# Optimization experiments

Hardware: AMD Instinct MI355X
Metric: run time of the kernel (lower is better)

Reference implementation:

```python
import jax, jax.numpy as jnp
import numpy as np

B, S, E, H = 4, 2048, 1024, 16
D = E // H  # head dim = 64
NEG = -1e9


def setup_inputs() -> dict:
    key = jax.random.key(0)
    ks = jax.random.split(key, 6)
    scale = 1.0 / np.sqrt(E)
    return {
        "x": jax.random.normal(ks[0], (B, S, E), dtype=jnp.float32),
        "in_proj_weight": jax.random.normal(ks[1], (3 * E, E), dtype=jnp.float32) * scale,
        "in_proj_bias": jax.random.normal(ks[2], (3 * E,), dtype=jnp.float32) * 0.02,
        "out_proj_weight": jax.random.normal(ks[3], (E, E), dtype=jnp.float32) * scale,
        "out_proj_bias": jax.random.normal(ks[4], (E,), dtype=jnp.float32) * 0.02,
        "mask": jax.random.randint(ks[5], (B, S), 0, 2, dtype=jnp.int32),
    }


def reference(x, in_proj_weight, in_proj_bias, out_proj_weight, out_proj_bias, mask):
    # Equivalent of F.multi_head_attention_forward(h,h,h,...) with batch-first x.
    # qkv projection: [B,S,3E]
    qkv = jnp.einsum("bse,fe->bsf", x, in_proj_weight) + in_proj_bias
    q, k, v = jnp.split(qkv, 3, axis=-1)
    # split heads -> [B,S,H,D]
    q = q.reshape(B, S, H, D) * (1.0 / np.sqrt(D))
    k = k.reshape(B, S, H, D)
    v = v.reshape(B, S, H, D)
    # scores [B,H,Sq,Sk]
    scores = jnp.einsum("bqhd,bkhd->bhqk", q, k)
    # key_padding_mask = (mask == 0): True positions are excluded
    pad = (mask == 0)[:, None, None, :]  # [B,1,1,Sk]
    scores = jnp.where(pad, NEG, scores)
    attn = jax.nn.softmax(scores, axis=-1)
    # attention output -> [B,S,E]
    ctx = jnp.einsum("bhqk,bkhd->bqhd", attn, v).reshape(B, S, E)
    h_ = jnp.einsum("bse,fe->bsf", ctx, out_proj_weight) + out_proj_bias
    # residual; dropout is identity in eval mode
    return x + h_
```

## Files before the change

kernel.cpp:

```cpp
#include <hip/hip_runtime.h>
#include <stdint.h>
#include <math.h>

#define B_ 4
#define S_ 2048
#define E_ 1024
#define H_ 16
#define D_ 64
#define M_ (B_*S_)

typedef __attribute__((ext_vector_type(8))) short bf16x8;
typedef __attribute__((ext_vector_type(4))) float f32x4;

__device__ __forceinline__ unsigned short f2bf(float f) {
  union { float f; uint32_t u; } v; v.f = f;
  uint32_t u = v.u;
  return (unsigned short)((u + 0x7FFFu + ((u >> 16) & 1u)) >> 16);
}

__device__ __forceinline__ void gload16(const void* g, void* l) {
  __builtin_amdgcn_global_load_lds(
      (__attribute__((address_space(1))) void*)g,
      (__attribute__((address_space(3))) void*)l, 16, 0, 0);
}

__device__ __forceinline__ uint32_t cvtpk(float lo, float hi) {
  uint32_t r;
  asm("v_cvt_pk_bf16_f32 %0, %1, %2" : "=v"(r) : "v"(lo), "v"(hi));
  return r;
}

#define N1 ((M_*E_)/4)
#define N2 ((3*E_*E_)/4)
#define N3 ((E_*E_)/4)
#define NM ((B_*S_)/4)
__global__ __launch_bounds__(256) void cvt_all(const float* __restrict__ x,
                                               const float* __restrict__ w1,
                                               const float* __restrict__ w2,
                                               const int* __restrict__ mask,
                                               unsigned short* __restrict__ dst,
                                               float* __restrict__ maskf) {
  int i = blockIdx.x * 256 + threadIdx.x;
  if (i < N1 + N2 + N3) {
    const float* src;
    int j;
    if (i < N1) { src = x; j = i; }
    else if (i < N1 + N2) { src = w1; j = i - N1; }
    else { src = w2; j = i - N1 - N2; }
    float4 v = reinterpret_cast<const float4*>(src)[j];
    ushort4 o;
    o.x = f2bf(v.x); o.y = f2bf(v.y); o.z = f2bf(v.z); o.w = f2bf(v.w);
    reinterpret_cast<ushort4*>(dst)[i] = o;
  } else if (i < N1 + N2 + N3 + NM) {
    int j = i - (N1 + N2 + N3);
    int4 m = reinterpret_cast<const int4*>(mask)[j];
    float4 o;
    o.x = m.x ? 0.0f : -2.0e9f;
    o.y = m.y ? 0.0f : -2.0e9f;
    o.z = m.z ? 0.0f : -2.0e9f;
    o.w = m.w ? 0.0f : -2.0e9f;
    reinterpret_cast<float4*>(maskf)[j] = o;
  }
}

__global__ __launch_bounds__(256) void gemm_qkv128(
    const unsigned short* __restrict__ A,
    const unsigned short* __restrict__ W,
    const float* __restrict__ bias,
    unsigned short* __restrict__ Qg,
    unsigned short* __restrict__ Kg,
    unsigned short* __restrict__ Vtg)
{
  __shared__ __align__(16) unsigned short SMEM[128*136];
  unsigned short* As = SMEM;
  unsigned short* Bs = SMEM + 4096;
  const int tid = threadIdx.x;
  const int lane = tid & 63;
  const int wave = tid >> 6;
  const int wm = (wave >> 1) * 64, wn = (wave & 1) * 64;
  const int l15 = lane & 15, lg = lane >> 4;

  const int orig = blockIdx.y * 24 + blockIdx.x;
  const int xcd = orig & 7;
  const int idx = orig >> 3;
  const int tn = (xcd * 3 + (idx % 3)) * 128;
  const int tm = (idx / 3) * 128;

  f32x4 zero4 = {0.f, 0.f, 0.f, 0.f};
  f32x4 acc[4][4];
  #pragma unroll
  for (int mi = 0; mi < 4; ++mi)
    #pragma unroll
    for (int ni = 0; ni < 4; ++ni) acc[mi][ni] = zero4;

  const int r0 = tid >> 2, c0 = (tid & 3) * 8;
  const unsigned short* Arow0 = A + (size_t)(tm + r0) * E_ + c0;
  const unsigned short* Arow1 = A + (size_t)(tm + r0 + 64) * E_ + c0;
  const unsigned short* Wrow0 = W + (size_t)(tn + r0) * E_ + c0;
  const unsigned short* Wrow1 = W + (size_t)(tn + r0 + 64) * E_ + c0;
  unsigned short* lA0 = As + tid * 8;
  unsigned short* lA1 = As + (tid + 256) * 8;
  unsigned short* lB0 = Bs + tid * 8;
  unsigned short* lB1 = Bs + (tid + 256) * 8;

  for (int k0 = 0; k0 < E_; k0 += 32) {
    gload16(Arow0 + k0, lA0);
    gload16(Arow1 + k0, lA1);
    gload16(Wrow0 + k0, lB0);
    gload16(Wrow1 + k0, lB1);
    __syncthreads();
    bf16x8 af[4], bfm[4];
    #pragma unroll
    for (int mi = 0; mi < 4; ++mi)
      af[mi] = *(const bf16x8*)&As[(wm + mi*16 + l15)*32 + lg*8];
    #pragma unroll
    for (int ni = 0; ni < 4; ++ni)
      bfm[ni] = *(const bf16x8*)&Bs[(wn + ni*16 + l15)*32 + lg*8];
    #pragma unroll
    for (int mi = 0; mi < 4; ++mi)
      #pragma unroll
      for (int ni = 0; ni < 4; ++ni)
        acc[mi][ni] = __builtin_amdgcn_mfma_f32_16x16x32_bf16(af[mi], bfm[ni], acc[mi][ni], 0, 0, 0);
    __syncthreads();
  }

  const int sec = tn >> 10;
  if (sec < 2) {
    #pragma unroll
    for (int ni = 0; ni < 4; ++ni) {
      const int col = tn + wn + ni*16 + l15;
      const float bcol = bias[col];
      const int f2 = col & 1023;
      const int h = f2 >> 6, d = f2 & 63;
      #pragma unroll
      for (int mi = 0; mi < 4; ++mi) {
        #pragma unroll
        for (int r = 0; r < 4; ++r) {
          const int row = tm + wm + mi*16 + lg*4 + r;
          const int b = row >> 11, s = row & (S_-1);
          const size_t bh = (size_t)(b * H_ + h);
          float val = acc[mi][ni][r] + bcol;
          if (sec == 0) {
            Qg[(bh*S_ + s)*D_ + d] = f2bf(val * 0.18033688f);
          } else {
            const int ch = (d >> 3) ^ (s & 7);
            Kg[(bh*S_ + s)*D_ + ch*8 + (d & 7)] = f2bf(val);
          }
        }
      }
    }
  } else {
    __syncthreads();
    unsigned short* T = SMEM;
    #pragma unroll
    for (int ni = 0; ni < 4; ++ni) {
      const int f = wn + ni*16 + l15;
      const float bcol = bias[tn + f];
      #pragma unroll
      for (int mi = 0; mi < 4; ++mi) {
        const int s0 = wm + mi*16 + lg*4;
        uint2 p;
        p.x = cvtpk(acc[mi][ni][0] + bcol, acc[mi][ni][1] + bcol);
        p.y = cvtpk(acc[mi][ni][2] + bcol, acc[mi][ni][3] + bcol);
        *reinterpret_cast<uint2*>(&T[f*136 + s0]) = p;
      }
    }
    __syncthreads();
    const int f = tid >> 1, sch = tid & 1;
    const int d = f & 63, hl = f >> 6;
    const int h = ((tn & 1023) >> 6) + hl;
    const int b = tm >> 11;
    const size_t bh = (size_t)(b * H_ + h);
    const int sbase = (tm & (S_-1)) + sch*64;
    unsigned short* vout = Vtg + (bh*D_ + d)*S_ + sbase;
    const unsigned short* tin = &T[f*136 + sch*64];
    #pragma unroll
    for (int j = 0; j < 8; ++j) {
      uint4 v = *reinterpret_cast<const uint4*>(&tin[j*8]);
      *reinterpret_cast<uint4*>(&vout[(j ^ (d & 7))*8]) = v;
    }
  }
}

__global__ __launch_bounds__(512, 4) void attn_fwd(
    const unsigned short* __restrict__ Qg,
    const unsigned short* __restrict__ Kg,
    const unsigned short* __restrict__ Vtg,
    const float* __restrict__ maskf,
    unsigned short* __restrict__ ctx)
{
  __shared__ __align__(16) unsigned short Ks[2][4096];
  __shared__ __align__(16) unsigned short Vs[2][4096];
  const int tid = threadIdx.x, lane = tid & 63, wave = tid >> 6;
  const int l15 = lane & 15, lg = lane >> 4;
  const int bh = blockIdx.y, b = bh >> 4, h = bh & 15;
  const int q0 = blockIdx.x * 256 + wave * 32;
  const unsigned short* Qb = Qg + (size_t)bh * S_ * D_;
  const unsigned short* Kb = Kg + (size_t)bh * S_ * D_;
  const unsigned short* Vb = Vtg + (size_t)bh * D_ * S_;
  const float* mrow = maskf + b * S_;

  bf16x8 qf[2][2];
  #pragma unroll
  for (int mi = 0; mi < 2; ++mi)
    #pragma unroll
    for (int kc = 0; kc < 2; ++kc)
      qf[mi][kc] = *(const bf16x8*)&Qb[(size_t)(q0 + mi*16 + l15)*D_ + kc*32 + lg*8];

  f32x4 zero4 = {0.f, 0.f, 0.f, 0.f};
  f32x4 accO[2][4];
  f32x4 accL[2] = {zero4, zero4};
  #pragma unroll
  for (int mi = 0; mi < 2; ++mi)
    #pragma unroll
    for (int df = 0; df < 4; ++df) accO[mi][df] = zero4;

  union { uint32_t u[4]; bf16x8 v; } ou;
  ou.u[0] = ou.u[1] = ou.u[2] = ou.u[3] = 0x3F803F80u;
  const bf16x8 onesv = ou.v;

  int kboff0[4], kboff1[4], vboff0[4], vboff1[4];
  #pragma unroll
  for (int kt = 0; kt < 4; ++kt) {
    const int krow = kt*16 + l15;
    kboff0[kt] = (krow*64 + ((lg ^ (krow & 7))*8)) * 2;
    kboff1[kt] = (krow*64 + (((4+lg) ^ (krow & 7))*8)) * 2;
  }
  #pragma unroll
  for (int df = 0; df < 4; ++df) {
    const int vrow = df*16 + l15;
    vboff0[df] = (vrow*64 + ((lg ^ (vrow & 7))*8)) * 2;
    vboff1[df] = (vrow*64 + (((4+lg) ^ (vrow & 7))*8)) * 2;
  }
  const char* KsB = (const char*)&Ks[0][0];
  const char* VsB = (const char*)&Vs[0][0];

  const int sr0 = tid >> 3, sc0 = (tid & 7) * 8;

  gload16(Kb + (size_t)sr0 * D_ + sc0, &Ks[0][tid*8]);
  gload16(Vb + (size_t)sr0 * S_ + sc0, &Vs[0][tid*8]);
  f32x4 mv0[4], mv1[4];
  #pragma unroll
  for (int kt = 0; kt < 4; ++kt)
    mv0[kt] = *(const f32x4*)&mrow[kt*16 + lg*4];
  const unsigned short* kpre = Kb + (size_t)(64 + sr0) * D_ + sc0;
  const unsigned short* vpre = Vb + (size_t)sr0 * S_ + 64 + sc0;
  const float* mpre = mrow + 64 + lg*4;
  __syncthreads();

#define ATTN_TILE(CUR, MVC, MVN, DO_PF)                                         \
  {                                                                             \
    if (DO_PF) {                                                                \
      gload16(kpre, &Ks[(CUR)^1][tid*8]);                                       \
      gload16(vpre, &Vs[(CUR)^1][tid*8]);                                       \
      kpre += 64*D_; vpre += 64;                                                \
      _Pragma("unroll")                                                         \
      for (int kt = 0; kt < 4; ++kt)                                            \
        MVN[kt] = *(const f32x4*)&mpre[kt*16];                                  \
      mpre += 64;                                                               \
    }                                                                           \
    f32x4 s_[2][4];                                                             \
    __builtin_amdgcn_s_setprio(1);                                              \
    _Pragma("unroll")                                                           \
    for (int kt = 0; kt < 4; ++kt) {                                            \
      bf16x8 kf0 = *(const bf16x8*)(KsB + (CUR)*8192 + kboff0[kt]);             \
      bf16x8 kf1 = *(const bf16x8*)(KsB + (CUR)*8192 + kboff1[kt]);             \
      s_[0][kt] = __builtin_amdgcn_mfma_f32_16x16x32_bf16(kf0, qf[0][0], MVC[kt], 0, 0, 0); \
      s_[0][kt] = __builtin_amdgcn_mfma_f32_16x16x32_bf16(kf1, qf[0][1], s_[0][kt], 0, 0, 0); \
      s_[1][kt] = __builtin_amdgcn_mfma_f32_16x16x32_bf16(kf0, qf[1][0], MVC[kt], 0, 0, 0); \
      s_[1][kt] = __builtin_amdgcn_mfma_f32_16x16x32_bf16(kf1, qf[1][1], s_[1][kt], 0, 0, 0); \
    }                                                                           \
    __builtin_amdgcn_s_setprio(0);                                              \
    _Pragma("unroll")                                                           \
    for (int mi = 0; mi < 2; ++mi)                                              \
      _Pragma("unroll")                                                         \
      for (int kt = 0; kt < 4; ++kt)                                            \
        _Pragma("unroll")                                                       \
        for (int r = 0; r < 4; ++r)                                             \
          s_[mi][kt][r] = __builtin_amdgcn_exp2f(s_[mi][kt][r]);                \
    bf16x8 pa[2][2];                                                            \
    _Pragma("unroll")                                                           \
    for (int mi = 0; mi < 2; ++mi) {                                            \
      _Pragma("unroll")                                                         \
      for (int kk = 0; kk < 2; ++kk) {                                          \
        uint32_t a0 = cvtpk(s_[mi][2*kk][0],   s_[mi][2*kk][1]);                \
        uint32_t c1 = cvtpk(s_[mi][2*kk][2],   s_[mi][2*kk][3]);                \
        uint32_t b0 = cvtpk(s_[mi][2*kk+1][0], s_[mi][2*kk+1][1]);              \
        uint32_t d1 = cvtpk(s_[mi][2*kk+1][2], s_[mi][2*kk+1][3]);              \
        asm("v_permlane32_swap_b32 %0, %1" : "+v"(a0), "+v"(b0));               \
        asm("v_permlane16_swap_b32 %0, %1" : "+v"(a0), "+v"(b0));               \
        asm("v_permlane32_swap_b32 %0, %1" : "+v"(c1), "+v"(d1));               \
        asm("v_permlane16_swap_b32 %0, %1" : "+v"(c1), "+v"(d1));               \
        union { bf16x8 v; uint32_t u[4]; } w;                                   \
        w.u[0] = a0; w.u[1] = c1; w.u[2] = b0; w.u[3] = d1;                     \
        pa[mi][kk] = w.v;                                                       \
      }                                                                         \
    }                                                                           \
    __builtin_amdgcn_s_setprio(1);                                              \
    accL[0] = __builtin_amdgcn_mfma_f32_16x16x32_bf16(pa[0][0], onesv, accL[0], 0, 0, 0); \
    accL[1] = __builtin_amdgcn_mfma_f32_16x16x32_bf16(pa[1][0], onesv, accL[1], 0, 0, 0); \
    _Pragma("unroll")                                                           \
    for (int df = 0; df < 4; ++df) {                                            \
      bf16x8 vf = *(const bf16x8*)(VsB + (CUR)*8192 + vboff0[df]);              \
      accO[0][df] = __builtin_amdgcn_mfma_f32_16x16x32_bf16(pa[0][0], vf, accO[0][df], 0, 0, 0); \
      accO[1][df] = __builtin_amdgcn_mfma_f32_16x16x32_bf16(pa[1][0], vf, accO[1][df], 0, 0, 0); \
    }                                                                           \
    accL[0] = __builtin_amdgcn_mfma_f32_16x16x32_bf16(pa[0][1], onesv, accL[0], 0, 0, 0); \
    accL[1] = __builtin_amdgcn_mfma_f32_16x16x32_bf16(pa[1][1], onesv, accL[1], 0, 0, 0); \
    _Pragma("unroll")                                                           \
    for (int df = 0; df < 4; ++df) {                                            \
      bf16x8 vf = *(const bf16x8*)(VsB + (CUR)*8192 + vboff1[df]);              \
      accO[0][df] = __builtin_amdgcn_mfma_f32_16x16x32_bf16(pa[0][1], vf, accO[0][df], 0, 0, 0); \
      accO[1][df] = __builtin_amdgcn_mfma_f32_16x16x32_bf16(pa[1][1], vf, accO[1][df], 0, 0, 0); \
    }                                                                           \
    __builtin_amdgcn_s_setprio(0);                                              \
    __syncthreads();                                                            \
  }

  for (int tt = 0; tt < 32; tt += 2) {
    ATTN_TILE(0, mv0, mv1, 1)
    ATTN_TILE(1, mv1, mv0, (tt < 30))
  }
#undef ATTN_TILE

  #pragma unroll
  for (int mi = 0; mi < 2; ++mi) {
    #pragma unroll
    for (int r = 0; r < 4; ++r) {
      const float iv = 1.0f / accL[mi][r];
      const int srow = q0 + mi*16 + lg*4 + r;
      #pragma unroll
      for (int df = 0; df < 4; ++df) {
        const int d = df*16 + l15;
        ctx[((size_t)b*S_ + srow)*E_ + h*D_ + d] = f2bf(accO[mi][df][r] * iv);
      }
    }
  }
}

__global__ __launch_bounds__(256) void gemm_out(
    const unsigned short* __restrict__ A,
    const unsigned short* __restrict__ W,
    const float* __restrict__ bias,
    const float* __restrict__ xres,
    float* __restrict__ out)
{
  __shared__ __align__(16) unsigned short As[128*32];
  __shared__ __align__(16) unsigned short Bs[128*32];
  const int tid = threadIdx.x;
  const int lane = tid & 63;
  const int wave = tid >> 6;
  const int wm = (wave >> 1) * 64, wn = (wave & 1) * 64;
  const int tm = blockIdx.y * 128, tn = blockIdx.x * 128;
  const int l15 = lane & 15, lg = lane >> 4;

  f32x4 zero4 = {0.f, 0.f, 0.f, 0.f};
  f32x4 acc[4][4];
  #pragma unroll
  for (int mi = 0; mi < 4; ++mi)
    #pragma unroll
    for (int ni = 0; ni < 4; ++ni) acc[mi][ni] = zero4;

  const int r0 = tid >> 2, c0 = (tid & 3) * 8;
  const unsigned short* Arow0 = A + (size_t)(tm + r0) * E_ + c0;
  const unsigned short* Arow1 = A + (size_t)(tm + r0 + 64) * E_ + c0;
  const unsigned short* Wrow0 = W + (size_t)(tn + r0) * E_ + c0;
  const unsigned short* Wrow1 = W + (size_t)(tn + r0 + 64) * E_ + c0;
  unsigned short* lA0 = As + tid * 8;
  unsigned short* lA1 = As + (tid + 256) * 8;
  unsigned short* lB0 = Bs + tid * 8;
  unsigned short* lB1 = Bs + (tid + 256) * 8;

  for (int k0 = 0; k0 < E_; k0 += 32) {
    gload16(Arow0 + k0, lA0);
    gload16(Arow1 + k0, lA1);
    gload16(Wrow0 + k0, lB0);
    gload16(Wrow1 + k0, lB1);
    __syncthreads();
    bf16x8 af[4], bfm[4];
    #pragma unroll
    for (int mi = 0; mi < 4; ++mi)
      af[mi] = *(const bf16x8*)&As[(wm + mi*16 + l15)*32 + lg*8];
    #pragma unroll
    for (int ni = 0; ni < 4; ++ni)
      bfm[ni] = *(const bf16x8*)&Bs[(wn + ni*16 + l15)*32 + lg*8];
    #pragma unroll
    for (int mi = 0; mi < 4; ++mi)
      #pragma unroll
      for (int ni = 0; ni < 4; ++ni)
        acc[mi][ni] = __builtin_amdgcn_mfma_f32_16x16x32_bf16(af[mi], bfm[ni], acc[mi][ni], 0, 0, 0);
    __syncthreads();
  }

  #pragma unroll
  for (int ni = 0; ni < 4; ++ni) {
    const int col = tn + wn + ni*16 + l15;
    const float bcol = bias[col];
    #pragma unroll
    for (int mi = 0; mi < 4; ++mi) {
      #pragma unroll
      for (int r = 0; r < 4; ++r) {
        const int row = tm + wm + mi*16 + lg*4 + r;
        out[(size_t)row*E_ + col] = xres[(size_t)row*E_ + col] + acc[mi][ni][r] + bcol;
      }
    }
  }
}

extern "C" void kernel_launch(void* const* d_in, const int* in_sizes, int n_in,
                              void* d_out, int out_size, void* d_ws, size_t ws_size,
                              hipStream_t stream) {
  const float* x  = (const float*)d_in[0];
  const float* w1 = (const float*)d_in[1];
  const float* b1 = (const float*)d_in[2];
  const float* w2 = (const float*)d_in[3];
  const float* b2 = (const float*)d_in[4];
  const int* mask = (const int*)d_in[5];
  float* out = (float*)d_out;

  const size_t SZ = (size_t)B_*H_*S_*D_;
  unsigned short* Qg  = (unsigned short*)d_ws;
  unsigned short* Kg  = Qg + SZ;
  unsigned short* Vtg = Kg + SZ;
  unsigned short* xb  = Vtg + SZ;
  unsigned short* w1b = xb + (size_t)M_*E_;
  unsigned short* w2b = w1b + (size_t)3*E_*E_;
  float* maskf = (float*)(w2b + (size_t)E_*E_);
  unsigned short* ctx = xb;

  const int ntot = N1 + N2 + N3 + NM;
  cvt_all<<<(ntot + 255)/256, 256, 0, stream>>>(x, w1, w2, mask, xb, maskf);

  gemm_qkv128<<<dim3(24, 64), 256, 0, stream>>>(xb, w1b, b1, Qg, Kg, Vtg);
  attn_fwd<<<dim3(S_/256, B_*H_), 512, 0, stream>>>(Qg, Kg, Vtg, maskf, ctx);
  gemm_out<<<dim3(E_/128, M_/128), 256, 0, stream>>>(ctx, w2b, b2, x, out);
}
```

Baseline: 226.4 us.

## Stage attention output through LDS for coalesced stores and remap blocks across XCDs

The attention epilogue now writes normalized bf16 outputs into a padded per-wave LDS tile and then stores 16-byte vectors per lane, replacing the scattered 2-byte global writes. The grid becomes 1D and the block index is remapped so that the 8 query tiles of one batch-head land on the same XCD under round-robin dispatch, improving L2 reuse of K/V. Shared memory grows to 36 KB to hold the staging buffer, which may affect occupancy under launch_bounds(512,4).

```diff
diff --git a/kernel.cpp b/kernel.cpp
--- a/kernel.cpp
+++ b/kernel.cpp
@@ -189,12 +189,18 @@
     const float* __restrict__ maskf,
     unsigned short* __restrict__ ctx)
 {
-  __shared__ __align__(16) unsigned short Ks[2][4096];
-  __shared__ __align__(16) unsigned short Vs[2][4096];
+  __shared__ __align__(16) unsigned char SMEM[36864];
+  unsigned short* KsP = (unsigned short*)SMEM;
+  unsigned short* VsP = (unsigned short*)(SMEM + 16384);
   const int tid = threadIdx.x, lane = tid & 63, wave = tid >> 6;
   const int l15 = lane & 15, lg = lane >> 4;
-  const int bh = blockIdx.y, b = bh >> 4, h = bh & 15;
-  const int q0 = blockIdx.x * 256 + wave * 32;
+
+  const int lin = blockIdx.x;
+  const int bh = (lin & 7) * 8 + (lin >> 6);
+  const int qi = (lin >> 3) & 7;
+  const int b = bh >> 4, h = bh & 15;
+  const int q0 = qi * 256 + wave * 32;
+
   const unsigned short* Qb = Qg + (size_t)bh * S_ * D_;
   const unsigned short* Kb = Kg + (size_t)bh * S_ * D_;
   const unsigned short* Vb = Vtg + (size_t)bh * D_ * S_;
@@ -232,13 +238,13 @@
     vboff0[df] = (vrow*64 + ((lg ^ (vrow & 7))*8)) * 2;
     vboff1[df] = (vrow*64 + (((4+lg) ^ (vrow & 7))*8)) * 2;
   }
-  const char* KsB = (const char*)&Ks[0][0];
-  const char* VsB = (const char*)&Vs[0][0];
+  const char* KsB = (const char*)KsP;
+  const char* VsB = (const char*)VsP;
 
   const int sr0 = tid >> 3, sc0 = (tid & 7) * 8;
 
-  gload16(Kb + (size_t)sr0 * D_ + sc0, &Ks[0][tid*8]);
-  gload16(Vb + (size_t)sr0 * S_ + sc0, &Vs[0][tid*8]);
+  gload16(Kb + (size_t)sr0 * D_ + sc0, KsP + tid*8);
+  gload16(Vb + (size_t)sr0 * S_ + sc0, VsP + tid*8);
   f32x4 mv0[4], mv1[4];
   #pragma unroll
   for (int kt = 0; kt < 4; ++kt)
@@ -251,8 +257,8 @@
 #define ATTN_TILE(CUR, MVC, MVN, DO_PF)                                         \
   {                                                                             \
     if (DO_PF) {                                                                \
-      gload16(kpre, &Ks[(CUR)^1][tid*8]);                                       \
-      gload16(vpre, &Vs[(CUR)^1][tid*8]);                                       \
+      gload16(kpre, KsP + ((CUR)^1)*4096 + tid*8);                              \
+      gload16(vpre, VsP + ((CUR)^1)*4096 + tid*8);                              \
       kpre += 64*D_; vpre += 64;                                                \
       _Pragma("unroll")                                                         \
       for (int kt = 0; kt < 4; ++kt)                                            \
@@ -323,17 +329,28 @@
   }
 #undef ATTN_TILE
 
+  unsigned short* T = (unsigned short*)SMEM + wave * 2304;
   #pragma unroll
   for (int mi = 0; mi < 2; ++mi) {
     #pragma unroll
     for (int r = 0; r < 4; ++r) {
       const float iv = 1.0f / accL[mi][r];
-      const int srow = q0 + mi*16 + lg*4 + r;
-      #pragma unroll
-      for (int df = 0; df < 4; ++df) {
-        const int d = df*16 + l15;
-        ctx[((size_t)b*S_ + srow)*E_ + h*D_ + d] = f2bf(accO[mi][df][r] * iv);
-      }
+      const int q = mi*16 + lg*4 + r;
+      #pragma unroll
+      for (int df = 0; df < 4; ++df)
+        T[q*72 + df*16 + l15] = f2bf(accO[mi][df][r] * iv);
+    }
+  }
+  __syncthreads();
+  {
+    const int g = lane >> 2, c4 = lane & 3;
+    #pragma unroll
+    for (int j = 0; j < 4; ++j) {
+      const int t = j*16 + g;
+      const int q = t >> 1, half = t & 1;
+      uint4 v = *reinterpret_cast<const uint4*>(&T[q*72 + half*32 + c4*8]);
+      const int srow = q0 + q;
+      *reinterpret_cast<uint4*>(&ctx[((size_t)b*S_ + srow)*E_ + h*D_ + half*32 + c4*8]) = v;
     }
   }
 }
@@ -432,6 +449,6 @@
   cvt_all<<<(ntot + 255)/256, 256, 0, stream>>>(x, w1, w2, mask, xb, maskf);
 
   gemm_qkv128<<<dim3(24, 64), 256, 0, stream>>>(xb, w1b, b1, Qg, Kg, Vtg);
-  attn_fwd<<<dim3(S_/256, B_*H_), 512, 0, stream>>>(Qg, Kg, Vtg, maskf, ctx);
+  attn_fwd<<<512, 512, 0, stream>>>(Qg, Kg, Vtg, maskf, ctx);
   gemm_out<<<dim3(E_/128, M_/128), 256, 0, stream>>>(ctx, w2b, b2, x, out);
 }
```

New measurement: 210.2 us. 7.1% less time.
